# Kernel optimization log

Hardware: AMD Instinct MI355X
Metric: run time of the kernel (lower is better)

The kernel has to match this reference:

```python
import jax, jax.numpy as jnp
import numpy as np

SEQ_LEN = 256
HIDDEN = 1024
OUT = 1024
BATCH = 256


def setup_inputs() -> dict:
    key = jax.random.key(0)
    ks = jax.random.split(key, 7)
    s = 0.02
    return {
        "c_vector": jax.random.normal(ks[0], (BATCH, HIDDEN), dtype=jnp.float32),
        # PyTorch LSTM weights, gate order (i, f, g, o)
        "W_ih": jax.random.normal(ks[1], (4 * HIDDEN, OUT), dtype=jnp.float32) * s,
        "W_hh": jax.random.normal(ks[2], (4 * HIDDEN, HIDDEN), dtype=jnp.float32) * s,
        "b_ih": jax.random.normal(ks[3], (4 * HIDDEN,), dtype=jnp.float32) * s,
        "b_hh": jax.random.normal(ks[4], (4 * HIDDEN,), dtype=jnp.float32) * s,
        "W_fc": jax.random.normal(ks[5], (OUT, HIDDEN), dtype=jnp.float32) * s,
        "b_fc": jax.random.normal(ks[6], (OUT,), dtype=jnp.float32) * s,
    }


def reference(c_vector, W_ih, W_hh, b_ih, b_hh, W_fc, b_fc):
    bs = c_vector.shape[0]

    def step(carry, _):
        i_t, h, c = carry
        # fused gate GEMM: [bs, 4H]
        gates = i_t @ W_ih.T + b_ih + h @ W_hh.T + b_hh
        i_g, f_g, g_g, o_g = jnp.split(gates, 4, axis=-1)
        c_new = jax.nn.sigmoid(f_g) * c + jax.nn.sigmoid(i_g) * jnp.tanh(g_g)
        h_new = jax.nn.sigmoid(o_g) * jnp.tanh(c_new)
        # note: original applies fc_out to the CELL state, and feeds it back as input
        o_t = c_new @ W_fc.T + b_fc
        return (o_t, h_new, c_new), (h_new, c_new, o_t)

    i0 = jnp.zeros((bs, OUT), dtype=c_vector.dtype)
    init = (i0, c_vector, c_vector)
    _, (hs, cs, outs) = jax.lax.scan(step, init, None, length=SEQ_LEN)
    # scan stacks along time first: [T, bs, D] -> [bs, T, D]
    h_states = jnp.transpose(hs, (1, 0, 2))
    c_states = jnp.transpose(cs, (1, 0, 2))
    outputs = jnp.transpose(outs, (1, 0, 2))
    return (h_states, c_states, outputs)
```

## Files before the change

### kernel.cpp

```cpp
#include <hip/hip_runtime.h>

#define T_STEPS 256
#define NBATCH  256
#define HID     1024
#define KTOT    2048

typedef short bf16x8 __attribute__((ext_vector_type(8)));
typedef float f32x4  __attribute__((ext_vector_type(4)));

__device__ inline short cvt_bf16(float f) {
  unsigned u = __builtin_bit_cast(unsigned, f);
  u += 0x7fffu + ((u >> 16) & 1u);
  return (short)(u >> 16);
}

__device__ inline float fast_sigmoid(float x) {
  return __builtin_amdgcn_rcpf(1.0f + __builtin_amdgcn_exp2f(-1.44269504f * x));
}
__device__ inline float fast_tanh(float x) {
  return 2.0f * __builtin_amdgcn_rcpf(1.0f + __builtin_amdgcn_exp2f(-2.88539008f * x)) - 1.0f;
}

__global__ void cast_kernel(const float* __restrict__ Whh,
                            const float* __restrict__ Wfc,
                            const float* __restrict__ cvec,
                            short* __restrict__ Wbig,
                            short* __restrict__ Wfcb,
                            short* __restrict__ x0) {
  long i = (long)blockIdx.x * blockDim.x + threadIdx.x;
  const long nWhh = 4096L * 1024 / 4;
  const long nWfc = 1024L * 1024 / 4;
  const long nX0  = 256L * KTOT / 4;
  if (i < nWhh) {
    int up = (int)(i >> 8);
    int c4 = ((int)i & 255) * 4;
    int g = (up >> 4) & 3, ug = up >> 6, uu = up & 15;
    int in_row = g * 1024 + ug * 16 + uu;
    float4 v = *(const float4*)(Whh + (long)in_row * 1024 + c4);
    short4 o;
    o.x = cvt_bf16(v.x); o.y = cvt_bf16(v.y); o.z = cvt_bf16(v.z); o.w = cvt_bf16(v.w);
    *(short4*)(Wbig + (long)up * KTOT + 1024 + c4) = o;
  } else if (i < nWhh + nWfc) {
    long q = i - nWhh;
    float4 v = ((const float4*)Wfc)[q];
    short4 o;
    o.x = cvt_bf16(v.x); o.y = cvt_bf16(v.y); o.z = cvt_bf16(v.z); o.w = cvt_bf16(v.w);
    *(short4*)(Wfcb + q * 4) = o;
  } else if (i < nWhh + nWfc + nX0) {
    long q = i - nWhh - nWfc;
    int m = (int)(q >> 9);
    int c4 = ((int)q & 511) * 4;
    short4 o;
    if (c4 < 1024) {
      o.x = o.y = o.z = o.w = 0;
    } else {
      float4 v = *(const float4*)(cvec + (long)m * 1024 + (c4 - 1024));
      o.x = cvt_bf16(v.x); o.y = cvt_bf16(v.y); o.z = cvt_bf16(v.z); o.w = cvt_bf16(v.w);
    }
    *(short4*)(x0 + (long)m * KTOT + c4) = o;
  }
}

__global__ void bias_kernel(const float* __restrict__ W_ih,
                            const float* __restrict__ b_ih,
                            const float* __restrict__ b_hh,
                            const float* __restrict__ b_fc,
                            float* __restrict__ b0r, float* __restrict__ bcr) {
  int w = threadIdx.x >> 6, l = threadIdx.x & 63;
  int n = blockIdx.x * 4 + w;
  const float* row = W_ih + (long)n * HID;
  float s = 0.f;
  for (int i = l; i < HID; i += 64) s += row[i] * b_fc[i];
  #pragma unroll
  for (int off = 32; off; off >>= 1) s += __shfl_xor(s, off, 64);
  if (l == 0) {
    int g = n >> 10, uidx = n & 1023, ug = uidx >> 4, uu = uidx & 15;
    int up = ug * 64 + g * 16 + uu;
    float base = b_ih[n] + b_hh[n];
    b0r[up] = base;
    bcr[up] = base + s;
  }
}

__global__ void wc_kernel(const float* __restrict__ W_ih,
                          const float* __restrict__ W_fc,
                          short* __restrict__ Wbig) {
  int w = threadIdx.x >> 6, l = threadIdx.x & 63;
  int tile = blockIdx.x * 4 + w;
  int nt = tile >> 6, kt = tile & 63;
  int lr = l & 15, lq = l >> 4;
  f32x4 acc = {0.f, 0.f, 0.f, 0.f};
  const float* arow = W_ih + (long)(nt * 16 + lr) * HID + lq * 8;
  const float* bcol = W_fc + (long)(lq * 8) * HID + kt * 16 + lr;
  for (int jc = 0; jc < HID; jc += 32) {
    float4 a0 = *(const float4*)(arow + jc);
    float4 a1 = *(const float4*)(arow + jc + 4);
    bf16x8 a;
    a[0]=cvt_bf16(a0.x); a[1]=cvt_bf16(a0.y); a[2]=cvt_bf16(a0.z); a[3]=cvt_bf16(a0.w);
    a[4]=cvt_bf16(a1.x); a[5]=cvt_bf16(a1.y); a[6]=cvt_bf16(a1.z); a[7]=cvt_bf16(a1.w);
    bf16x8 b;
    #pragma unroll
    for (int jj = 0; jj < 8; ++jj) b[jj] = cvt_bf16(bcol[(long)(jc + jj) * HID]);
    acc = __builtin_amdgcn_mfma_f32_16x16x32_bf16(a, b, acc, 0, 0, 0);
  }
  int k = kt * 16 + lr;
  int g = nt >> 6, ug = nt & 63;
  #pragma unroll
  for (int r = 0; r < 4; ++r) {
    int up = ug * 64 + g * 16 + lq * 4 + r;
    Wbig[(long)up * KTOT + k] = cvt_bf16(acc[r]);
  }
}

__global__ __launch_bounds__(256, 1)
void step_kernel(int t,
                 const short* __restrict__ x,
                 const short* __restrict__ Wbig,
                 const float* __restrict__ bias,
                 const float* __restrict__ cprev,
                 long cprev_rs,
                 float* __restrict__ hst, float* __restrict__ cst,
                 short* __restrict__ xnext) {
  int tid = threadIdx.x;
  int w = tid >> 6, l = tid & 63, lr = l & 15, lq = l >> 4;
  int b = blockIdx.x;
  int ug = (b & 7) * 8 + ((b >> 3) & 7);
  int mg = b >> 6;

  const short* abase = x    + (long)(mg * 64 + lr) * KTOT + w * 512 + lq * 8;
  const short* bbase = Wbig + (long)(ug * 64 + lr) * KTOT + w * 512 + lq * 8;

  f32x4 acc[4][4] = {};
  #pragma unroll 2
  for (int kk = 0; kk < 512; kk += 32) {
    bf16x8 af[4], bfr[4];
    #pragma unroll
    for (int i = 0; i < 4; ++i) {
      af[i]  = *(const bf16x8*)(abase + (long)i * 16 * KTOT + kk);
      bfr[i] = *(const bf16x8*)(bbase + (long)i * 16 * KTOT + kk);
    }
    #pragma unroll
    for (int mi = 0; mi < 4; ++mi)
      #pragma unroll
      for (int ui = 0; ui < 4; ++ui)
        acc[mi][ui] = __builtin_amdgcn_mfma_f32_16x16x32_bf16(af[mi], bfr[ui], acc[mi][ui], 0, 0, 0);
  }

  __shared__ f32x4 lds4[4 * 4 * 4 * 64];
  #pragma unroll
  for (int mi = 0; mi < 4; ++mi)
    if (mi != w) {
      #pragma unroll
      for (int ui = 0; ui < 4; ++ui)
        lds4[((w * 4 + mi) * 4 + ui) * 64 + l] = acc[mi][ui];
    }
  __syncthreads();
  f32x4 red[4];
  #pragma unroll
  for (int ui = 0; ui < 4; ++ui) {
    red[ui] = acc[w][ui];
    #pragma unroll
    for (int wv = 0; wv < 4; ++wv)
      if (wv != w) red[ui] += lds4[((wv * 4 + w) * 4 + ui) * 64 + l];
  }

  int unit = ug * 16 + lr;
  float bi = bias[ug * 64 +  0 + lr];
  float bff= bias[ug * 64 + 16 + lr];
  float bg = bias[ug * 64 + 32 + lr];
  float bo = bias[ug * 64 + 48 + lr];
  #pragma unroll
  for (int r = 0; r < 4; ++r) {
    int m = mg * 64 + w * 16 + lq * 4 + r;
    float c_old = cprev[(long)m * cprev_rs + unit];
    float ig = fast_sigmoid(red[0][r] + bi);
    float fg = fast_sigmoid(red[1][r] + bff);
    float gg = fast_tanh(red[2][r] + bg);
    float og = fast_sigmoid(red[3][r] + bo);
    float cn = fg * c_old + ig * gg;
    float hn = og * fast_tanh(cn);
    long o = ((long)m * T_STEPS + t) * HID + unit;
    hst[o] = hn;
    cst[o] = cn;
    xnext[(long)m * KTOT + unit]        = cvt_bf16(cn);
    xnext[(long)m * KTOT + 1024 + unit] = cvt_bf16(hn);
  }
}

__global__ void fc_kernel(const float* __restrict__ A,
                          const short* __restrict__ Bw,
                          const float* __restrict__ b_fc,
                          float* __restrict__ out) {
  int w = threadIdx.x >> 6, l = threadIdx.x & 63;
  int wave = blockIdx.x * 4 + w;
  int ut = wave & 15, mt = wave >> 4;
  int lr = l & 15, lq = l >> 4;
  f32x4 acc[4][4] = {};
  const float* arow[4]; const short* brow[4];
  #pragma unroll
  for (int i = 0; i < 4; ++i) {
    arow[i] = A  + (long)(mt * 64 + i * 16 + lr) * HID + lq * 8;
    brow[i] = Bw + (long)(ut * 64 + i * 16 + lr) * HID + lq * 8;
  }
  for (int kc = 0; kc < HID; kc += 32) {
    bf16x8 a[4], b[4];
    #pragma unroll
    for (int i = 0; i < 4; ++i) {
      float4 v0 = *(const float4*)(arow[i] + kc);
      float4 v1 = *(const float4*)(arow[i] + kc + 4);
      bf16x8 r;
      r[0]=cvt_bf16(v0.x); r[1]=cvt_bf16(v0.y); r[2]=cvt_bf16(v0.z); r[3]=cvt_bf16(v0.w);
      r[4]=cvt_bf16(v1.x); r[5]=cvt_bf16(v1.y); r[6]=cvt_bf16(v1.z); r[7]=cvt_bf16(v1.w);
      a[i] = r;
      b[i] = *(const bf16x8*)(brow[i] + kc);
    }
    #pragma unroll
    for (int mi = 0; mi < 4; ++mi)
      #pragma unroll
      for (int ui = 0; ui < 4; ++ui)
        acc[mi][ui] = __builtin_amdgcn_mfma_f32_16x16x32_bf16(a[mi], b[ui], acc[mi][ui], 0, 0, 0);
  }
  int u0 = ut * 64;
  #pragma unroll
  for (int ui = 0; ui < 4; ++ui) {
    float bf = b_fc[u0 + ui * 16 + lr];
    #pragma unroll
    for (int mi = 0; mi < 4; ++mi)
      #pragma unroll
      for (int r = 0; r < 4; ++r) {
        long mo = (long)mt * 64 + mi * 16 + lq * 4 + r;
        out[mo * HID + u0 + ui * 16 + lr] = acc[mi][ui][r] + bf;
      }
  }
}

extern "C" void kernel_launch(void* const* d_in, const int* in_sizes, int n_in,
                              void* d_out, int out_size, void* d_ws, size_t ws_size,
                              hipStream_t stream) {
  const float* cvec = (const float*)d_in[0];
  const float* W_ih = (const float*)d_in[1];
  const float* W_hh = (const float*)d_in[2];
  const float* b_ih = (const float*)d_in[3];
  const float* b_hh = (const float*)d_in[4];
  const float* W_fc = (const float*)d_in[5];
  const float* b_fc = (const float*)d_in[6];
  float* out = (float*)d_out;
  float* hst = out;
  float* cst = out + (long)NBATCH * T_STEPS * HID;
  float* ost = out + 2L * NBATCH * T_STEPS * HID;

  char* base = (char*)d_ws;
  size_t off = 0;
  auto carve = [&](size_t bytes) -> char* {
    char* r = base + off;
    off = (off + bytes + 255) & ~(size_t)255;
    return r;
  };
  short* Wbig = (short*)carve(4096L * KTOT * 2);
  short* Wfcb = (short*)carve(1024L * 1024 * 2);
  float* b0r  = (float*)carve(4096 * 4);
  float* bcr  = (float*)carve(4096 * 4);
  short* xb[2];
  xb[0] = (short*)carve((long)NBATCH * KTOT * 2);
  xb[1] = (short*)carve((long)NBATCH * KTOT * 2);

  cast_kernel<<<5632, 256, 0, stream>>>(W_hh, W_fc, cvec, Wbig, Wfcb, xb[0]);
  bias_kernel<<<1024, 256, 0, stream>>>(W_ih, b_ih, b_hh, b_fc, b0r, bcr);
  wc_kernel<<<4096, 256, 0, stream>>>(W_ih, W_fc, Wbig);

  for (int t = 0; t < T_STEPS; ++t) {
    const float* cprev = (t == 0) ? cvec : (cst + (long)(t - 1) * HID);
    long cprev_rs = (t == 0) ? (long)HID : (long)T_STEPS * HID;
    const float* bias = (t == 0) ? b0r : bcr;
    step_kernel<<<256, 256, 0, stream>>>(t, xb[t & 1], Wbig, bias,
                                         cprev, cprev_rs, hst, cst,
                                         xb[(t + 1) & 1]);
  }
  fc_kernel<<<4096, 256, 0, stream>>>(cst, Wfcb, b_fc, ost);
}
```

Before: 7.868 ms.

## Pre-swizzle weights and activations into MFMA fragment order, use 8-wave K-split step kernel

Stores Wbig and the per-step input buffer in a tiled layout that matches the MFMA fragment order, so each lane loads a contiguous 16-byte chunk and the global loads coalesce fully. The step kernel goes from 4 to 8 waves, each covering a 256-wide K slice. It gains register double-buffered prefetch, a two-stage LDS reduction, and hoisted loads of bias and c_old. Output stores become nontemporal. The cost is more complex index arithmetic and an extra barrier plus LDS round trip in the reduction.

```diff
diff --git a/kernel.cpp b/kernel.cpp
--- a/kernel.cpp
+++ b/kernel.cpp
@@ -20,6 +20,7 @@
 __device__ inline float fast_tanh(float x) {
   return 2.0f * __builtin_amdgcn_rcpf(1.0f + __builtin_amdgcn_exp2f(-2.88539008f * x)) - 1.0f;
 }
+
 
 __global__ void cast_kernel(const float* __restrict__ Whh,
                             const float* __restrict__ Wfc,
@@ -32,14 +33,16 @@
   const long nWfc = 1024L * 1024 / 4;
   const long nX0  = 256L * KTOT / 4;
   if (i < nWhh) {
-    int up = (int)(i >> 8);
+    int in_row = (int)(i >> 8);
     int c4 = ((int)i & 255) * 4;
-    int g = (up >> 4) & 3, ug = up >> 6, uu = up & 15;
-    int in_row = g * 1024 + ug * 16 + uu;
+    int g = in_row >> 10, rem = in_row & 1023, ug = rem >> 4, uu = rem & 15;
+    int k = 1024 + c4;
+    int k32 = k >> 5, kq = (k >> 3) & 3, j = k & 7;
     float4 v = *(const float4*)(Whh + (long)in_row * 1024 + c4);
     short4 o;
     o.x = cvt_bf16(v.x); o.y = cvt_bf16(v.y); o.z = cvt_bf16(v.z); o.w = cvt_bf16(v.w);
-    *(short4*)(Wbig + (long)up * KTOT + 1024 + c4) = o;
+    long dst = ((((long)(ug * 64 + k32) * 4 + g) * 64) + kq * 16 + uu) * 8 + j;
+    *(short4*)(Wbig + dst) = o;
   } else if (i < nWhh + nWfc) {
     long q = i - nWhh;
     float4 v = ((const float4*)Wfc)[q];
@@ -57,7 +60,10 @@
       float4 v = *(const float4*)(cvec + (long)m * 1024 + (c4 - 1024));
       o.x = cvt_bf16(v.x); o.y = cvt_bf16(v.y); o.z = cvt_bf16(v.z); o.w = cvt_bf16(v.w);
     }
-    *(short4*)(x0 + (long)m * KTOT + c4) = o;
+    int k32 = c4 >> 5, kq = (c4 >> 3) & 3, j = c4 & 7;
+    int mtile = m >> 4, mrow = m & 15;
+    long dst = (((long)mtile * 64 + k32) * 64 + kq * 16 + mrow) * 8 + j;
+    *(short4*)(x0 + dst) = o;
   }
 }
 
@@ -105,14 +111,15 @@
   }
   int k = kt * 16 + lr;
   int g = nt >> 6, ug = nt & 63;
+  int k32 = k >> 5, kq = (k >> 3) & 3, j = k & 7;
   #pragma unroll
   for (int r = 0; r < 4; ++r) {
-    int up = ug * 64 + g * 16 + lq * 4 + r;
-    Wbig[(long)up * KTOT + k] = cvt_bf16(acc[r]);
-  }
-}
-
-__global__ __launch_bounds__(256, 1)
+    long dst = ((((long)(ug * 64 + k32) * 4 + g) * 64) + kq * 16 + (lq * 4 + r)) * 8 + j;
+    Wbig[dst] = cvt_bf16(acc[r]);
+  }
+}
+
+__global__ __launch_bounds__(512, 2)
 void step_kernel(int t,
                  const short* __restrict__ x,
                  const short* __restrict__ Wbig,
@@ -127,63 +134,98 @@
   int ug = (b & 7) * 8 + ((b >> 3) & 7);
   int mg = b >> 6;
 
-  const short* abase = x    + (long)(mg * 64 + lr) * KTOT + w * 512 + lq * 8;
-  const short* bbase = Wbig + (long)(ug * 64 + lr) * KTOT + w * 512 + lq * 8;
+  int unit = ug * 16 + lr;
+  float c_old[4], bi = 0.f, bff = 0.f, bg = 0.f, bo = 0.f;
+  if (w < 4) {
+    bi  = bias[ug * 64 +  0 + lr];
+    bff = bias[ug * 64 + 16 + lr];
+    bg  = bias[ug * 64 + 32 + lr];
+    bo  = bias[ug * 64 + 48 + lr];
+    #pragma unroll
+    for (int r = 0; r < 4; ++r) {
+      int m = mg * 64 + w * 16 + lq * 4 + r;
+      c_old[r] = cprev[(long)m * cprev_rs + unit];
+    }
+  }
+
+  const short* ab = x    + ((long)(mg * 4) * 64 + w * 8) * 512 + l * 8;
+  const short* bb = Wbig + ((long)(ug * 64 + w * 8) * 4) * 512 + l * 8;
 
   f32x4 acc[4][4] = {};
-  #pragma unroll 2
-  for (int kk = 0; kk < 512; kk += 32) {
-    bf16x8 af[4], bfr[4];
-    #pragma unroll
-    for (int i = 0; i < 4; ++i) {
-      af[i]  = *(const bf16x8*)(abase + (long)i * 16 * KTOT + kk);
-      bfr[i] = *(const bf16x8*)(bbase + (long)i * 16 * KTOT + kk);
+  bf16x8 af[2][4], bfr[2][4];
+  #pragma unroll
+  for (int i = 0; i < 4; ++i) {
+    af[0][i]  = *(const bf16x8*)(ab + (long)i * 32768);
+    bfr[0][i] = *(const bf16x8*)(bb + (long)i * 512);
+  }
+  #pragma unroll
+  for (int it = 0; it < 8; ++it) {
+    const int cur = it & 1, nxt = cur ^ 1;
+    if (it < 7) {
+      #pragma unroll
+      for (int i = 0; i < 4; ++i) {
+        af[nxt][i]  = *(const bf16x8*)(ab + (long)(it + 1) * 512 + (long)i * 32768);
+        bfr[nxt][i] = *(const bf16x8*)(bb + (long)(it + 1) * 2048 + (long)i * 512);
+      }
     }
     #pragma unroll
     for (int mi = 0; mi < 4; ++mi)
       #pragma unroll
       for (int ui = 0; ui < 4; ++ui)
-        acc[mi][ui] = __builtin_amdgcn_mfma_f32_16x16x32_bf16(af[mi], bfr[ui], acc[mi][ui], 0, 0, 0);
+        acc[mi][ui] = __builtin_amdgcn_mfma_f32_16x16x32_bf16(af[cur][mi], bfr[cur][ui], acc[mi][ui], 0, 0, 0);
   }
 
   __shared__ f32x4 lds4[4 * 4 * 4 * 64];
-  #pragma unroll
-  for (int mi = 0; mi < 4; ++mi)
-    if (mi != w) {
+  if (w >= 4) {
+    #pragma unroll
+    for (int mi = 0; mi < 4; ++mi)
       #pragma unroll
       for (int ui = 0; ui < 4; ++ui)
-        lds4[((w * 4 + mi) * 4 + ui) * 64 + l] = acc[mi][ui];
-    }
+        lds4[(((w - 4) * 4 + mi) * 4 + ui) * 64 + l] = acc[mi][ui];
+  }
   __syncthreads();
-  f32x4 red[4];
-  #pragma unroll
-  for (int ui = 0; ui < 4; ++ui) {
-    red[ui] = acc[w][ui];
-    #pragma unroll
-    for (int wv = 0; wv < 4; ++wv)
-      if (wv != w) red[ui] += lds4[((wv * 4 + w) * 4 + ui) * 64 + l];
-  }
-
-  int unit = ug * 16 + lr;
-  float bi = bias[ug * 64 +  0 + lr];
-  float bff= bias[ug * 64 + 16 + lr];
-  float bg = bias[ug * 64 + 32 + lr];
-  float bo = bias[ug * 64 + 48 + lr];
-  #pragma unroll
-  for (int r = 0; r < 4; ++r) {
-    int m = mg * 64 + w * 16 + lq * 4 + r;
-    float c_old = cprev[(long)m * cprev_rs + unit];
-    float ig = fast_sigmoid(red[0][r] + bi);
-    float fg = fast_sigmoid(red[1][r] + bff);
-    float gg = fast_tanh(red[2][r] + bg);
-    float og = fast_sigmoid(red[3][r] + bo);
-    float cn = fg * c_old + ig * gg;
-    float hn = og * fast_tanh(cn);
-    long o = ((long)m * T_STEPS + t) * HID + unit;
-    hst[o] = hn;
-    cst[o] = cn;
-    xnext[(long)m * KTOT + unit]        = cvt_bf16(cn);
-    xnext[(long)m * KTOT + 1024 + unit] = cvt_bf16(hn);
+  if (w < 4) {
+    #pragma unroll
+    for (int mi = 0; mi < 4; ++mi)
+      #pragma unroll
+      for (int ui = 0; ui < 4; ++ui) {
+        acc[mi][ui] += lds4[((w * 4 + mi) * 4 + ui) * 64 + l];
+        if (mi != w)
+          lds4[((w * 4 + mi) * 4 + ui) * 64 + l] = acc[mi][ui];
+      }
+  }
+  __syncthreads();
+  if (w < 4) {
+    f32x4 red[4];
+    #pragma unroll
+    for (int ui = 0; ui < 4; ++ui) {
+      red[ui] = acc[w][ui];
+      #pragma unroll
+      for (int wv = 0; wv < 4; ++wv)
+        if (wv != w) red[ui] += lds4[((wv * 4 + w) * 4 + ui) * 64 + l];
+    }
+
+    int mtile = mg * 4 + w;
+    int k32c = ug >> 1;
+    int kqc = (ug & 1) * 2 + (lr >> 3);
+    int jc = lr & 7;
+    long xbase = ((((long)mtile * 64 + k32c) * 64) + kqc * 16) * 8 + jc;
+    #pragma unroll
+    for (int r = 0; r < 4; ++r) {
+      int m = mg * 64 + w * 16 + lq * 4 + r;
+      float ig = fast_sigmoid(red[0][r] + bi);
+      float fg = fast_sigmoid(red[1][r] + bff);
+      float gg = fast_tanh(red[2][r] + bg);
+      float og = fast_sigmoid(red[3][r] + bo);
+      float cn = fg * c_old[r] + ig * gg;
+      float hn = og * fast_tanh(cn);
+      long o = ((long)m * T_STEPS + t) * HID + unit;
+      __builtin_nontemporal_store(hn, &hst[o]);
+      __builtin_nontemporal_store(cn, &cst[o]);
+      int mrow = lq * 4 + r;
+      xnext[xbase + (long)mrow * 8]         = cvt_bf16(cn);
+      xnext[xbase + (long)mrow * 8 + 16384] = cvt_bf16(hn);
+    }
   }
 }
 
@@ -229,7 +271,8 @@
       #pragma unroll
       for (int r = 0; r < 4; ++r) {
         long mo = (long)mt * 64 + mi * 16 + lq * 4 + r;
-        out[mo * HID + u0 + ui * 16 + lr] = acc[mi][ui][r] + bf;
+        __builtin_nontemporal_store(acc[mi][ui][r] + bf,
+                                    &out[mo * HID + u0 + ui * 16 + lr]);
       }
   }
 }
@@ -272,7 +315,7 @@
     const float* cprev = (t == 0) ? cvec : (cst + (long)(t - 1) * HID);
     long cprev_rs = (t == 0) ? (long)HID : (long)T_STEPS * HID;
     const float* bias = (t == 0) ? b0r : bcr;
-    step_kernel<<<256, 256, 0, stream>>>(t, xb[t & 1], Wbig, bias,
+    step_kernel<<<256, 512, 0, stream>>>(t, xb[t & 1], Wbig, bias,
                                          cprev, cprev_rs, hst, cst,
                                          xb[(t + 1) & 1]);
   }
```

Result: slower. 8.613 ms (+9.5%).
